# Kernel optimization log

Hardware: AMD Instinct MI355X
Metric: run time of the kernel (lower is better)

## Reference

```python
import jax, jax.numpy as jnp
import numpy as np

B, D, H, NSTEPS = 4096, 512, 2048, 16


def setup_inputs() -> dict:
    key = jax.random.key(0)
    k1, k2, k3, k4 = jax.random.split(key, 4)
    s_x = 1.0 / np.sqrt(D)
    s_h = 1.0 / np.sqrt(H)
    return {
        "z_in": jax.random.normal(k1, (B, D), dtype=jnp.float32),
        "Wx": jax.random.normal(k2, (D, H), dtype=jnp.float32) * s_x,
        "Wh": jax.random.normal(k3, (H, H), dtype=jnp.float32) * s_h,
        "bh": jnp.zeros((H,), dtype=jnp.float32),
        "Wout": jax.random.normal(k4, (H, D), dtype=jnp.float32) * s_h,
        "bout": jnp.zeros((D,), dtype=jnp.float32),
        "n_steps": NSTEPS,
    }


def reference(z_in, Wx, Wh, bh, Wout, bout, n_steps):
    # Input projection is identical every step (same z_in fed each iteration).
    xproj = z_in @ Wx + bh  # [B, H]
    h0 = jnp.zeros((z_in.shape[0], Wh.shape[0]), dtype=z_in.dtype)

    def step(h, _):
        h_new = jnp.tanh(xproj + h @ Wh)          # Elman RNN cell, hidden retained
        out = h_new @ Wout + bout                  # MLP head hidden -> latent
        return h_new, out

    _, outs = jax.lax.scan(step, h0, None, length=n_steps)  # [n_steps, B, D]
    return jnp.transpose(outs, (1, 0, 2))  # torch.stack(outs, 1) -> [B, n_steps, D]
```

## Files before the change

### kernel.cpp

```cpp
#include <hip/hip_runtime.h>
#include <hip/hip_bf16.h>
#include <stdint.h>

#define B_ 4096
#define D_ 512
#define H_ 2048
#define NS_ 16

typedef __bf16 bf16x8 __attribute__((ext_vector_type(8)));
typedef float f32x4 __attribute__((ext_vector_type(4)));
typedef short short4v __attribute__((ext_vector_type(4)));
typedef __attribute__((address_space(3))) const bf16x8* lds_frag_p;

__device__ __forceinline__ short f2bf(float f) {
  union { float f; uint32_t u; } c; c.f = f;
  uint32_t u = c.u;
  return (short)((u + 0x7fffu + ((u >> 16) & 1u)) >> 16);
}

__device__ __forceinline__ float tanh_fast(float x) {
  float e = __expf(2.0f * x);
  return 1.0f - 2.0f / (e + 1.0f);
}

__device__ __forceinline__ void gload16(const void* g, void* l) {
  __builtin_amdgcn_global_load_lds((const __attribute__((address_space(1))) void*)g,
                                   (__attribute__((address_space(3))) void*)l,
                                   16, 0, 0);
}

__global__ __launch_bounds__(256, 3) void gemm128_fused(
    const short* __restrict__ A, const short* __restrict__ Bt, int K,
    const float* __restrict__ xproj, const float* __restrict__ bias,
    float* __restrict__ outf, short* __restrict__ outh, int tout, int gridN)
{
  __shared__ short lds[3 * 8192];
  const int tid = threadIdx.x, lane = tid & 63, wid = tid >> 6;
  const int wm = wid >> 1, wn = wid & 1;

  const int nwg = gridDim.x;
  const int cpx = nwg >> 3;
  const int swz = ((int)blockIdx.x & 7) * cpx + ((int)blockIdx.x >> 3);
  const int tm = swz / gridN, tn = swz % gridN;
  const int row0 = tm * 128, col0 = tn * 128;

  const int NT = K >> 5;

  const int r0 = wid * 16 + (lane >> 2);
  const int r1 = r0 + 64;
  const int sl = lane & 3;
  const short* gA0 = A  + (size_t)(row0 + r0) * K + ((sl ^ ((r0 >> 1) & 3)) << 3);
  const short* gA1 = A  + (size_t)(row0 + r1) * K + ((sl ^ ((r1 >> 1) & 3)) << 3);
  const short* gB0 = Bt + (size_t)(col0 + r0) * K + ((sl ^ ((r0 >> 1) & 3)) << 3);
  const short* gB1 = Bt + (size_t)(col0 + r1) * K + ((sl ^ ((r1 >> 1) & 3)) << 3);
  const int dls = (wid * 16 + (lane >> 2)) * 32 + (lane & 3) * 8;

  const int rr = lane & 15, s4 = lane >> 4;
  int offA[4], offB[4];
#pragma unroll
  for (int m = 0; m < 4; ++m) {
    int r = wm * 64 + m * 16 + rr;
    offA[m] = r * 32 + ((s4 ^ ((r >> 1) & 3)) << 3);
  }
#pragma unroll
  for (int n = 0; n < 4; ++n) {
    int r = wn * 64 + n * 16 + rr;
    offB[n] = 4096 + r * 32 + ((s4 ^ ((r >> 1) & 3)) << 3);
  }

  f32x4 acc[4][4];
#pragma unroll
  for (int m = 0; m < 4; ++m)
#pragma unroll
    for (int n = 0; n < 4; ++n)
      acc[m][n] = (f32x4){0.f, 0.f, 0.f, 0.f};

  auto stage = [&](int kt, int base) {
    const size_t ko = (size_t)kt * 32;
    gload16(gA0 + ko, &lds[base + dls]);
    gload16(gA1 + ko, &lds[base + 2048 + dls]);
    gload16(gB0 + ko, &lds[base + 4096 + dls]);
    gload16(gB1 + ko, &lds[base + 6144 + dls]);
  };

  stage(0, 0);
  stage(1, 8192);
  asm volatile("s_waitcnt vmcnt(4)" ::: "memory");
  __builtin_amdgcn_s_barrier();

  int cur = 0, stb = 2;
  for (int kt = 0; kt < NT; ++kt) {
    const bool st = (kt + 2 < NT);
    if (st) {
      stage(kt + 2, stb * 8192);
      stb = (stb == 2) ? 0 : stb + 1;
    }
    const int bb = cur * 8192;

    bf16x8 a[4], b[4];
#pragma unroll
    for (int m = 0; m < 4; ++m) a[m] = *(lds_frag_p)&lds[bb + offA[m]];
#pragma unroll
    for (int n = 0; n < 4; ++n) b[n] = *(lds_frag_p)&lds[bb + offB[n]];

#pragma unroll
    for (int m = 0; m < 4; ++m)
#pragma unroll
      for (int n = 0; n < 4; ++n)
        acc[m][n] = __builtin_amdgcn_mfma_f32_16x16x32_bf16(a[m], b[n], acc[m][n], 0, 0, 0);

    if (st) {
      asm volatile("s_waitcnt vmcnt(4)" ::: "memory");
    } else if (kt == NT - 2) {
      asm volatile("s_waitcnt vmcnt(0)" ::: "memory");
    }
    if (kt < NT - 1) __builtin_amdgcn_s_barrier();
    cur = (cur == 2) ? 0 : cur + 1;
  }

  const int rb = row0 + wm * 64 + ((lane >> 4) << 2);
  const int cb = col0 + wn * 64 + (lane & 15);
#pragma unroll
  for (int m = 0; m < 4; ++m) {
#pragma unroll
    for (int n = 0; n < 4; ++n) {
      const int col = cb + n * 16;
#pragma unroll
      for (int r = 0; r < 4; ++r) {
        const int row = rb + m * 16 + r;
        float v = acc[m][n][r];
        if (col < H_) {
          float x = xproj[(size_t)row * H_ + col];
          outh[(size_t)row * H_ + col] = f2bf(tanh_fast(x + v));
        } else {
          int oc = col - H_;
          outf[(size_t)row * (NS_ * D_) + tout * D_ + oc] = v + bias[oc];
        }
      }
    }
  }
}

template<int BM, int BN, int EPI>
__global__ __launch_bounds__(256, 2) void gemm_bt(
    const short* __restrict__ A, const short* __restrict__ Bt, int K,
    const float* __restrict__ xproj, const float* __restrict__ bias,
    float* __restrict__ outf, short* __restrict__ outh, int ldN, int tout)
{
  constexpr int WM = BM / 2, WN = BN / 2;
  constexpr int RM = WM / 16, RN = WN / 16;
  __shared__ short lds[2][(BM + BN) * 32];
  const int tid = threadIdx.x, lane = tid & 63, wid = tid >> 6;
  const int wm = wid >> 1, wn = wid & 1;
  const int row0 = blockIdx.y * BM, col0 = blockIdx.x * BN;
  const short* Ag = A + (size_t)row0 * K;
  const short* Bg = Bt + (size_t)col0 * K;

  f32x4 acc[RM][RN];
#pragma unroll
  for (int m = 0; m < RM; ++m)
#pragma unroll
    for (int n = 0; n < RN; ++n)
      acc[m][n] = (f32x4){0.f, 0.f, 0.f, 0.f};

  const int nt = K >> 5;

  auto stage = [&](int kt, int buf) {
    const short* ga = Ag + (kt << 5);
#pragma unroll
    for (int i = 0; i < BM * 4; i += 256) {
      int slot = i + tid;
      gload16(ga + (size_t)(slot >> 2) * K + ((slot & 3) << 3), &lds[buf][slot * 8]);
    }
    const short* gb = Bg + (kt << 5);
#pragma unroll
    for (int i = 0; i < BN * 4; i += 256) {
      int slot = i + tid;
      gload16(gb + (size_t)(slot >> 2) * K + ((slot & 3) << 3),
              &lds[buf][BM * 32 + slot * 8]);
    }
  };

  stage(0, 0);
  __syncthreads();
  int cur = 0;
  const int kq = (lane >> 4) << 3;
  const int rr = lane & 15;
  for (int kt = 0; kt < nt; ++kt) {
    if (kt + 1 < nt) stage(kt + 1, cur ^ 1);
    const short* la = &lds[cur][(wm * WM) * 32];
    const short* lb = &lds[cur][BM * 32 + (wn * WN) * 32];
    bf16x8 a[RM], b[RN];
#pragma unroll
    for (int m = 0; m < RM; ++m)
      a[m] = *(const bf16x8*)(la + (m * 16 + rr) * 32 + kq);
#pragma unroll
    for (int n = 0; n < RN; ++n)
      b[n] = *(const bf16x8*)(lb + (n * 16 + rr) * 32 + kq);
#pragma unroll
    for (int m = 0; m < RM; ++m)
#pragma unroll
      for (int n = 0; n < RN; ++n)
        acc[m][n] = __builtin_amdgcn_mfma_f32_16x16x32_bf16(a[m], b[n], acc[m][n], 0, 0, 0);
    __syncthreads();
    cur ^= 1;
  }

  const int rb = row0 + wm * WM + ((lane >> 4) << 2);
  const int cb = col0 + wn * WN + (lane & 15);
#pragma unroll
  for (int m = 0; m < RM; ++m) {
#pragma unroll
    for (int n = 0; n < RN; ++n) {
      const int col = cb + n * 16;
#pragma unroll
      for (int r = 0; r < 4; ++r) {
        const int row = rb + m * 16 + r;
        float v = acc[m][n][r];
        if (EPI == 0) {
          outf[(size_t)row * ldN + col] = v + bias[col];
        } else {
          outf[(size_t)row * (NS_ * D_) + tout * D_ + col] = v + bias[col];
        }
      }
    }
  }
}

__global__ void transpose_cvt(const float* __restrict__ in, short* __restrict__ out,
                              int R, int C) {
  __shared__ float tile[32][33];
  const int tx = threadIdx.x & 31, ty = threadIdx.x >> 5;
  const int c0 = blockIdx.x * 32, r0 = blockIdx.y * 32;
#pragma unroll
  for (int i = 0; i < 32; i += 8)
    tile[ty + i][tx] = in[(size_t)(r0 + ty + i) * C + c0 + tx];
  __syncthreads();
#pragma unroll
  for (int i = 0; i < 32; i += 8)
    out[(size_t)(c0 + ty + i) * R + r0 + tx] = f2bf(tile[tx][ty + i]);
}

__global__ void cvt_bf16_k(const float4* __restrict__ in, short4v* __restrict__ out, int n4) {
  int i = blockIdx.x * 256 + threadIdx.x;
  if (i >= n4) return;
  float4 v = in[i];
  short4v o;
  o[0] = f2bf(v.x); o[1] = f2bf(v.y); o[2] = f2bf(v.z); o[3] = f2bf(v.w);
  out[i] = o;
}

__global__ void tanh_h0_k(const float4* __restrict__ xp, short4v* __restrict__ h, int n4) {
  int i = blockIdx.x * 256 + threadIdx.x;
  if (i >= n4) return;
  float4 v = xp[i];
  short4v o;
  o[0] = f2bf(tanh_fast(v.x)); o[1] = f2bf(tanh_fast(v.y));
  o[2] = f2bf(tanh_fast(v.z)); o[3] = f2bf(tanh_fast(v.w));
  h[i] = o;
}

extern "C" void kernel_launch(void* const* d_in, const int* in_sizes, int n_in,
                              void* d_out, int out_size, void* d_ws, size_t ws_size,
                              hipStream_t stream) {
  const float* z    = (const float*)d_in[0];
  const float* Wx   = (const float*)d_in[1];
  const float* Wh   = (const float*)d_in[2];
  const float* bh   = (const float*)d_in[3];
  const float* Wout = (const float*)d_in[4];
  const float* bout = (const float*)d_in[5];
  float* out = (float*)d_out;

  short* zb    = (short*)d_ws;
  short* WxT   = zb + (size_t)B_ * D_;
  short* WcatT = WxT + (size_t)H_ * D_;
  short* WoutT = WcatT + (size_t)H_ * H_;
  short* h0    = WcatT + (size_t)(H_ + D_) * H_;
  short* h1    = h0 + (size_t)B_ * H_;
  float* xproj = (float*)(h1 + (size_t)B_ * H_);

  cvt_bf16_k<<<(B_ * D_ / 4 + 255) / 256, 256, 0, stream>>>((const float4*)z, (short4v*)zb, B_ * D_ / 4);
  transpose_cvt<<<dim3(H_ / 32, D_ / 32), 256, 0, stream>>>(Wx, WxT, D_, H_);
  transpose_cvt<<<dim3(H_ / 32, H_ / 32), 256, 0, stream>>>(Wh, WcatT, H_, H_);
  transpose_cvt<<<dim3(D_ / 32, H_ / 32), 256, 0, stream>>>(Wout, WoutT, H_, D_);

  gemm_bt<128, 128, 0><<<dim3(H_ / 128, B_ / 128), 256, 0, stream>>>(
      zb, WxT, D_, nullptr, bh, xproj, nullptr, H_, 0);
  tanh_h0_k<<<(B_ * H_ / 4 + 255) / 256, 256, 0, stream>>>((const float4*)xproj, (short4v*)h0, B_ * H_ / 4);

  short* hb[2] = {h0, h1};
  for (int t = 1; t <= 15; ++t) {
    const short* hp = hb[(t - 1) & 1];
    short* hn = hb[t & 1];
    gemm128_fused<<<640, 256, 0, stream>>>(
        hp, WcatT, H_, xproj, bout, out, hn, t - 1, 20);
  }
  gemm_bt<128, 64, 2><<<dim3(D_ / 64, B_ / 128), 256, 0, stream>>>(
      hb[1], WoutT, H_, nullptr, bout, out, nullptr, 0, 15);
}
```

Measured before the change: 1.220 ms.

## Pre-pack recurrent weights into MFMA fragment layout and load B directly to registers

Adds a one-time kernel that packs Wh and Wout into a bf16 layout already arranged as MFMA B-fragments. The recurrent GEMM then reads B operands straight from global memory into registers, so only the A tile (hidden state) goes through LDS. The A tile uses a 4-stage LDS ring, and the k-loop double-buffers fragments in registers so the next step's loads overlap the current MFMAs. This removes the LDS traffic and staging for B. In exchange, B reads no longer share LDS reuse within the block, so they rely on cache hits, register pressure rises, and every iteration waits on lgkmcnt(0).

```diff
diff --git a/kernel.cpp b/kernel.cpp
--- a/kernel.cpp
+++ b/kernel.cpp
@@ -29,44 +29,42 @@
                                    16, 0, 0);
 }
 
-__global__ __launch_bounds__(256, 3) void gemm128_fused(
-    const short* __restrict__ A, const short* __restrict__ Bt, int K,
+__global__ __launch_bounds__(256, 3) void gemm128_fusedB(
+    const short* __restrict__ A, const short* __restrict__ Wfrag, int K,
     const float* __restrict__ xproj, const float* __restrict__ bias,
-    float* __restrict__ outf, short* __restrict__ outh, int tout, int gridN)
+    float* __restrict__ outf, short* __restrict__ outh, int tout)
 {
-  __shared__ short lds[3 * 8192];
+  __shared__ short lds[4 * 4096];
   const int tid = threadIdx.x, lane = tid & 63, wid = tid >> 6;
   const int wm = wid >> 1, wn = wid & 1;
-
-  const int nwg = gridDim.x;
-  const int cpx = nwg >> 3;
-  const int swz = ((int)blockIdx.x & 7) * cpx + ((int)blockIdx.x >> 3);
-  const int tm = swz / gridN, tn = swz % gridN;
+  const int NT = K >> 5;
+
+  const int g = ((int)blockIdx.x & 7) * 80 + ((int)blockIdx.x >> 3);
+  const int tm = g & 31, tn = g >> 5;
   const int row0 = tm * 128, col0 = tn * 128;
 
-  const int NT = K >> 5;
-
-  const int r0 = wid * 16 + (lane >> 2);
-  const int r1 = r0 + 64;
+  const int r0 = wid * 16 + (lane >> 2), r1 = r0 + 64;
   const int sl = lane & 3;
-  const short* gA0 = A  + (size_t)(row0 + r0) * K + ((sl ^ ((r0 >> 1) & 3)) << 3);
-  const short* gA1 = A  + (size_t)(row0 + r1) * K + ((sl ^ ((r1 >> 1) & 3)) << 3);
-  const short* gB0 = Bt + (size_t)(col0 + r0) * K + ((sl ^ ((r0 >> 1) & 3)) << 3);
-  const short* gB1 = Bt + (size_t)(col0 + r1) * K + ((sl ^ ((r1 >> 1) & 3)) << 3);
-  const int dls = (wid * 16 + (lane >> 2)) * 32 + (lane & 3) * 8;
+  const short* gA0 = A + (size_t)(row0 + r0) * K + ((sl ^ ((r0 >> 1) & 3)) << 3);
+  const short* gA1 = A + (size_t)(row0 + r1) * K + ((sl ^ ((r1 >> 1) & 3)) << 3);
+  const int dls = r0 * 32 + sl * 8;
+
+  auto stageA = [&](int kt) {
+    const int d = (kt & 3) * 4096 + dls;
+    const size_t ko = (size_t)kt * 32;
+    gload16(gA0 + ko, &lds[d]);
+    gload16(gA1 + ko, &lds[d + 2048]);
+  };
 
   const int rr = lane & 15, s4 = lane >> 4;
-  int offA[4], offB[4];
+  int offA[4];
 #pragma unroll
   for (int m = 0; m < 4; ++m) {
     int r = wm * 64 + m * 16 + rr;
     offA[m] = r * 32 + ((s4 ^ ((r >> 1) & 3)) << 3);
   }
-#pragma unroll
-  for (int n = 0; n < 4; ++n) {
-    int r = wn * 64 + n * 16 + rr;
-    offB[n] = 4096 + r * 32 + ((s4 ^ ((r >> 1) & 3)) << 3);
-  }
+
+  const short* bf = Wfrag + (size_t)(tn * 8 + wn * 4) * NT * 512 + lane * 8;
 
   f32x4 acc[4][4];
 #pragma unroll
@@ -75,47 +73,47 @@
     for (int n = 0; n < 4; ++n)
       acc[m][n] = (f32x4){0.f, 0.f, 0.f, 0.f};
 
-  auto stage = [&](int kt, int base) {
-    const size_t ko = (size_t)kt * 32;
-    gload16(gA0 + ko, &lds[base + dls]);
-    gload16(gA1 + ko, &lds[base + 2048 + dls]);
-    gload16(gB0 + ko, &lds[base + 4096 + dls]);
-    gload16(gB1 + ko, &lds[base + 6144 + dls]);
+  bf16x8 aX[4], bX[4], aY[4], bY[4];
+
+  stageA(0); stageA(1); stageA(2);
+#pragma unroll
+  for (int n = 0; n < 4; ++n) bX[n] = *(const bf16x8*)(bf + (size_t)n * NT * 512);
+  asm volatile("s_waitcnt vmcnt(0)" ::: "memory");
+  __builtin_amdgcn_s_barrier();
+#pragma unroll
+  for (int m = 0; m < 4; ++m) aX[m] = *(lds_frag_p)&lds[offA[m]];
+
+  auto iter = [&](int kt, bf16x8 (&ac)[4], bf16x8 (&bc)[4],
+                  bf16x8 (&an)[4], bf16x8 (&bn)[4]) {
+    const int kn = kt + 1;
+    if (kn < NT) {
+#pragma unroll
+      for (int n = 0; n < 4; ++n)
+        bn[n] = *(const bf16x8*)(bf + ((size_t)n * NT + kn) * 512);
+    }
+    if (kt + 3 < NT) stageA(kt + 3);
+    if (kn < NT) {
+      const int bb = (kn & 3) * 4096;
+#pragma unroll
+      for (int m = 0; m < 4; ++m) an[m] = *(lds_frag_p)&lds[bb + offA[m]];
+    }
+#pragma unroll
+    for (int m = 0; m < 4; ++m)
+#pragma unroll
+      for (int n = 0; n < 4; ++n)
+        acc[m][n] = __builtin_amdgcn_mfma_f32_16x16x32_bf16(ac[m], bc[n], acc[m][n], 0, 0, 0);
+    if (kt + 3 < NT) {
+      asm volatile("s_waitcnt vmcnt(2)" ::: "memory");
+    } else {
+      asm volatile("s_waitcnt vmcnt(0)" ::: "memory");
+    }
+    asm volatile("s_waitcnt lgkmcnt(0)" ::: "memory");
+    if (kt < NT - 1) __builtin_amdgcn_s_barrier();
   };
 
-  stage(0, 0);
-  stage(1, 8192);
-  asm volatile("s_waitcnt vmcnt(4)" ::: "memory");
-  __builtin_amdgcn_s_barrier();
-
-  int cur = 0, stb = 2;
-  for (int kt = 0; kt < NT; ++kt) {
-    const bool st = (kt + 2 < NT);
-    if (st) {
-      stage(kt + 2, stb * 8192);
-      stb = (stb == 2) ? 0 : stb + 1;
-    }
-    const int bb = cur * 8192;
-
-    bf16x8 a[4], b[4];
-#pragma unroll
-    for (int m = 0; m < 4; ++m) a[m] = *(lds_frag_p)&lds[bb + offA[m]];
-#pragma unroll
-    for (int n = 0; n < 4; ++n) b[n] = *(lds_frag_p)&lds[bb + offB[n]];
-
-#pragma unroll
-    for (int m = 0; m < 4; ++m)
-#pragma unroll
-      for (int n = 0; n < 4; ++n)
-        acc[m][n] = __builtin_amdgcn_mfma_f32_16x16x32_bf16(a[m], b[n], acc[m][n], 0, 0, 0);
-
-    if (st) {
-      asm volatile("s_waitcnt vmcnt(4)" ::: "memory");
-    } else if (kt == NT - 2) {
-      asm volatile("s_waitcnt vmcnt(0)" ::: "memory");
-    }
-    if (kt < NT - 1) __builtin_amdgcn_s_barrier();
-    cur = (cur == 2) ? 0 : cur + 1;
+  for (int kt = 0; kt < NT; kt += 2) {
+    iter(kt,     aX, bX, aY, bY);
+    iter(kt + 1, aY, bY, aX, bX);
   }
 
   const int rb = row0 + wm * 64 + ((lane >> 4) << 2);
@@ -139,6 +137,16 @@
       }
     }
   }
+}
+
+__global__ void wfrag_build(const float* __restrict__ Wh, const float* __restrict__ Wout,
+                            short* __restrict__ Wfrag) {
+  const int k = blockIdx.y;
+  const int col = blockIdx.x * 256 + threadIdx.x;
+  float v = (col < H_) ? Wh[(size_t)k * H_ + col]
+                       : Wout[(size_t)k * D_ + (col - H_)];
+  Wfrag[((size_t)(col >> 4) * 64 + (k >> 5)) * 512 +
+        ((k >> 3) & 3) * 128 + (col & 15) * 8 + (k & 7)] = f2bf(v);
 }
 
 template<int BM, int BN, int EPI>
@@ -273,16 +281,16 @@
 
   short* zb    = (short*)d_ws;
   short* WxT   = zb + (size_t)B_ * D_;
-  short* WcatT = WxT + (size_t)H_ * D_;
-  short* WoutT = WcatT + (size_t)H_ * H_;
-  short* h0    = WcatT + (size_t)(H_ + D_) * H_;
+  short* WoutT = WxT + (size_t)H_ * D_;
+  short* Wfrag = WoutT + (size_t)D_ * H_;
+  short* h0    = Wfrag + (size_t)(H_ + D_) * H_;
   short* h1    = h0 + (size_t)B_ * H_;
   float* xproj = (float*)(h1 + (size_t)B_ * H_);
 
   cvt_bf16_k<<<(B_ * D_ / 4 + 255) / 256, 256, 0, stream>>>((const float4*)z, (short4v*)zb, B_ * D_ / 4);
   transpose_cvt<<<dim3(H_ / 32, D_ / 32), 256, 0, stream>>>(Wx, WxT, D_, H_);
-  transpose_cvt<<<dim3(H_ / 32, H_ / 32), 256, 0, stream>>>(Wh, WcatT, H_, H_);
   transpose_cvt<<<dim3(D_ / 32, H_ / 32), 256, 0, stream>>>(Wout, WoutT, H_, D_);
+  wfrag_build<<<dim3((H_ + D_) / 256, H_), 256, 0, stream>>>(Wh, Wout, Wfrag);
 
   gemm_bt<128, 128, 0><<<dim3(H_ / 128, B_ / 128), 256, 0, stream>>>(
       zb, WxT, D_, nullptr, bh, xproj, nullptr, H_, 0);
@@ -292,8 +300,8 @@
   for (int t = 1; t <= 15; ++t) {
     const short* hp = hb[(t - 1) & 1];
     short* hn = hb[t & 1];
-    gemm128_fused<<<640, 256, 0, stream>>>(
-        hp, WcatT, H_, xproj, bout, out, hn, t - 1, 20);
+    gemm128_fusedB<<<640, 256, 0, stream>>>(
+        hp, Wfrag, H_, xproj, bout, out, hn, t - 1);
   }
   gemm_bt<128, 64, 2><<<dim3(D_ / 64, B_ / 128), 256, 0, stream>>>(
       hb[1], WoutT, H_, nullptr, bout, out, nullptr, 0, 15);
```

After: 1.261 ms. 3.3% more time.

## Shrink fused step GEMM tile to 128x64 with double buffering and more occupancy

Applied to the files above, without the earlier changes.

Replaces the 128x128 triple-buffered fused recurrence GEMM with a 128x64 tile kernel that uses two LDS buffers and plain __syncthreads, launched on 1280 workgroups with occupancy hint 5. The block-to-tile mapping is rewritten so groups of blocks share A rows, and the epilogue branches per block rather than per element. The aim is more waves in flight to hide latency and better balance across CUs. In exchange, per-tile arithmetic intensity drops, so A tiles are reloaded twice as often, and the shallower pipeline with full barriers may expose more memory latency.

```diff
diff --git a/kernel.cpp b/kernel.cpp
--- a/kernel.cpp
+++ b/kernel.cpp
@@ -29,22 +29,20 @@
                                    16, 0, 0);
 }
 
-__global__ __launch_bounds__(256, 3) void gemm128_fused(
+__global__ __launch_bounds__(256, 5) void fused_step(
     const short* __restrict__ A, const short* __restrict__ Bt, int K,
     const float* __restrict__ xproj, const float* __restrict__ bias,
-    float* __restrict__ outf, short* __restrict__ outh, int tout, int gridN)
+    float* __restrict__ outf, short* __restrict__ outh, int tout)
 {
-  __shared__ short lds[3 * 8192];
+  __shared__ short lds[2 * 6144];
   const int tid = threadIdx.x, lane = tid & 63, wid = tid >> 6;
   const int wm = wid >> 1, wn = wid & 1;
-
-  const int nwg = gridDim.x;
-  const int cpx = nwg >> 3;
-  const int swz = ((int)blockIdx.x & 7) * cpx + ((int)blockIdx.x >> 3);
-  const int tm = swz / gridN, tn = swz % gridN;
-  const int row0 = tm * 128, col0 = tn * 128;
-
   const int NT = K >> 5;
+
+  const int i = (int)blockIdx.x >> 3;
+  const int tn = ((int)blockIdx.x & 7) * 5 + (i % 5);
+  const int tm = i / 5;
+  const int row0 = tm * 128, col0 = tn * 64;
 
   const int r0 = wid * 16 + (lane >> 2);
   const int r1 = r0 + 64;
@@ -52,89 +50,79 @@
   const short* gA0 = A  + (size_t)(row0 + r0) * K + ((sl ^ ((r0 >> 1) & 3)) << 3);
   const short* gA1 = A  + (size_t)(row0 + r1) * K + ((sl ^ ((r1 >> 1) & 3)) << 3);
   const short* gB0 = Bt + (size_t)(col0 + r0) * K + ((sl ^ ((r0 >> 1) & 3)) << 3);
-  const short* gB1 = Bt + (size_t)(col0 + r1) * K + ((sl ^ ((r1 >> 1) & 3)) << 3);
-  const int dls = (wid * 16 + (lane >> 2)) * 32 + (lane & 3) * 8;
-
-  const int rr = lane & 15, s4 = lane >> 4;
-  int offA[4], offB[4];
-#pragma unroll
-  for (int m = 0; m < 4; ++m) {
-    int r = wm * 64 + m * 16 + rr;
-    offA[m] = r * 32 + ((s4 ^ ((r >> 1) & 3)) << 3);
-  }
-#pragma unroll
-  for (int n = 0; n < 4; ++n) {
-    int r = wn * 64 + n * 16 + rr;
-    offB[n] = 4096 + r * 32 + ((s4 ^ ((r >> 1) & 3)) << 3);
-  }
-
-  f32x4 acc[4][4];
-#pragma unroll
-  for (int m = 0; m < 4; ++m)
-#pragma unroll
-    for (int n = 0; n < 4; ++n)
-      acc[m][n] = (f32x4){0.f, 0.f, 0.f, 0.f};
+  const int dls = r0 * 32 + sl * 8;
 
   auto stage = [&](int kt, int base) {
     const size_t ko = (size_t)kt * 32;
     gload16(gA0 + ko, &lds[base + dls]);
     gload16(gA1 + ko, &lds[base + 2048 + dls]);
     gload16(gB0 + ko, &lds[base + 4096 + dls]);
-    gload16(gB1 + ko, &lds[base + 6144 + dls]);
   };
 
+  const int rr = lane & 15, s4 = lane >> 4;
+  int offA[4], offB[2];
+#pragma unroll
+  for (int m = 0; m < 4; ++m) {
+    int r = wm * 64 + m * 16 + rr;
+    offA[m] = r * 32 + ((s4 ^ ((r >> 1) & 3)) << 3);
+  }
+#pragma unroll
+  for (int n = 0; n < 2; ++n) {
+    int r = wn * 32 + n * 16 + rr;
+    offB[n] = 4096 + r * 32 + ((s4 ^ ((r >> 1) & 3)) << 3);
+  }
+
+  f32x4 acc[4][2];
+#pragma unroll
+  for (int m = 0; m < 4; ++m)
+#pragma unroll
+    for (int n = 0; n < 2; ++n)
+      acc[m][n] = (f32x4){0.f, 0.f, 0.f, 0.f};
+
   stage(0, 0);
-  stage(1, 8192);
-  asm volatile("s_waitcnt vmcnt(4)" ::: "memory");
-  __builtin_amdgcn_s_barrier();
-
-  int cur = 0, stb = 2;
+  __syncthreads();
   for (int kt = 0; kt < NT; ++kt) {
-    const bool st = (kt + 2 < NT);
-    if (st) {
-      stage(kt + 2, stb * 8192);
-      stb = (stb == 2) ? 0 : stb + 1;
-    }
-    const int bb = cur * 8192;
-
-    bf16x8 a[4], b[4];
+    if (kt + 1 < NT) stage(kt + 1, ((kt + 1) & 1) * 6144);
+    const int bb = (kt & 1) * 6144;
+    bf16x8 a[4], b[2];
 #pragma unroll
     for (int m = 0; m < 4; ++m) a[m] = *(lds_frag_p)&lds[bb + offA[m]];
 #pragma unroll
-    for (int n = 0; n < 4; ++n) b[n] = *(lds_frag_p)&lds[bb + offB[n]];
-
+    for (int n = 0; n < 2; ++n) b[n] = *(lds_frag_p)&lds[bb + offB[n]];
 #pragma unroll
     for (int m = 0; m < 4; ++m)
 #pragma unroll
-      for (int n = 0; n < 4; ++n)
+      for (int n = 0; n < 2; ++n)
         acc[m][n] = __builtin_amdgcn_mfma_f32_16x16x32_bf16(a[m], b[n], acc[m][n], 0, 0, 0);
-
-    if (st) {
-      asm volatile("s_waitcnt vmcnt(4)" ::: "memory");
-    } else if (kt == NT - 2) {
-      asm volatile("s_waitcnt vmcnt(0)" ::: "memory");
-    }
-    if (kt < NT - 1) __builtin_amdgcn_s_barrier();
-    cur = (cur == 2) ? 0 : cur + 1;
-  }
-
-  const int rb = row0 + wm * 64 + ((lane >> 4) << 2);
-  const int cb = col0 + wn * 64 + (lane & 15);
-#pragma unroll
-  for (int m = 0; m < 4; ++m) {
-#pragma unroll
-    for (int n = 0; n < 4; ++n) {
-      const int col = cb + n * 16;
-#pragma unroll
-      for (int r = 0; r < 4; ++r) {
-        const int row = rb + m * 16 + r;
-        float v = acc[m][n][r];
-        if (col < H_) {
+    __syncthreads();
+  }
+
+  const int rb = row0 + wm * 64 + (s4 << 2);
+  const int cb = col0 + wn * 32 + rr;
+  if (col0 < H_) {
+#pragma unroll
+    for (int m = 0; m < 4; ++m) {
+#pragma unroll
+      for (int n = 0; n < 2; ++n) {
+        const int col = cb + n * 16;
+#pragma unroll
+        for (int r = 0; r < 4; ++r) {
+          const int row = rb + m * 16 + r;
           float x = xproj[(size_t)row * H_ + col];
-          outh[(size_t)row * H_ + col] = f2bf(tanh_fast(x + v));
-        } else {
-          int oc = col - H_;
-          outf[(size_t)row * (NS_ * D_) + tout * D_ + oc] = v + bias[oc];
+          outh[(size_t)row * H_ + col] = f2bf(tanh_fast(x + acc[m][n][r]));
+        }
+      }
+    }
+  } else {
+#pragma unroll
+    for (int m = 0; m < 4; ++m) {
+#pragma unroll
+      for (int n = 0; n < 2; ++n) {
+        const int oc = cb - H_ + n * 16;
+#pragma unroll
+        for (int r = 0; r < 4; ++r) {
+          const int row = rb + m * 16 + r;
+          outf[(size_t)row * (NS_ * D_) + tout * D_ + oc] = acc[m][n][r] + bias[oc];
         }
       }
     }
@@ -292,8 +280,8 @@
   for (int t = 1; t <= 15; ++t) {
     const short* hp = hb[(t - 1) & 1];
     short* hn = hb[t & 1];
-    gemm128_fused<<<640, 256, 0, stream>>>(
-        hp, WcatT, H_, xproj, bout, out, hn, t - 1, 20);
+    fused_step<<<1280, 256, 0, stream>>>(
+        hp, WcatT, H_, xproj, bout, out, hn, t - 1);
   }
   gemm_bt<128, 64, 2><<<dim3(D_ / 64, B_ / 128), 256, 0, stream>>>(
       hb[1], WoutT, H_, nullptr, bout, out, nullptr, 0, 15);
```

New measurement: 1.199 ms. About the same (-1.8%).
